# Optimization experiments

Hardware: AMD Instinct MI355X
Metric: run time of the kernel (lower is better)

## Reference

```python
import jax, jax.numpy as jnp
import numpy as np


def setup_inputs() -> dict:
    key = jax.random.key(0)
    k1, k2, k3, k4, k5 = jax.random.split(key, 5)
    B, D, T = 32, 256, 32       # batch, word_feature_dim, seq_len
    Dh, H, Wd = 128, 128, 128   # image_feature_dim, height, width
    word_features = jax.random.normal(k1, (B, D, T), dtype=jnp.float32)
    image_features = jax.random.normal(k2, (B, Dh, H, Wd), dtype=jnp.float32)
    words_mask = jax.random.randint(k3, (B, T), 0, 2, dtype=jnp.int32)
    W = jax.random.normal(k4, (Dh, D), dtype=jnp.float32) * (1.0 / np.sqrt(D))
    b = jax.random.normal(k5, (Dh,), dtype=jnp.float32) * 0.01
    return {"word_features": word_features, "image_features": image_features,
            "words_mask": words_mask, "W": W, "b": b}


def reference(word_features, image_features, words_mask, W, b):
    B, D, T = word_features.shape
    Dh = image_features.shape[1]
    N = image_features.shape[2] * image_features.shape[3]  # H*W
    # values = fc(word_features^T)^T : [B, Dh, T]
    values = jnp.einsum('bdt,kd->bkt', word_features, W) + b[None, :, None]
    # queries: [B, N, Dh] (flatten spatial)
    queries = image_features.reshape(B, Dh, N)
    # scores S: [B, N, T]
    S = jnp.einsum('bkn,bkt->bnt', queries, values)
    mask = (words_mask != 0)[:, None, :]  # [B,1,T], True => masked
    S = jnp.where(mask, -jnp.inf, S)
    # softmax over seq dim (original: exp / sum(exp)); stable form is same math
    attn_coefficients = jax.nn.softmax(S, axis=2)  # [B, N, T]
    # context vectors: [B, Dh, N]
    attn = jnp.einsum('bkt,bnt->bkn', values, attn_coefficients)
    return attn, attn_coefficients
```

## Files before the change

### kernel.cpp

```cpp
#include <hip/hip_runtime.h>
#include <math.h>

constexpr int Bc  = 32;
constexpr int Dc  = 256;
constexpr int Tc  = 32;
constexpr int DHc = 128;
constexpr int Nc  = 16384;

__global__ __launch_bounds__(256) void values_kernel(
    const float* __restrict__ wf, const float* __restrict__ Wm,
    const float* __restrict__ bias, float* __restrict__ values)
{
    int id = blockIdx.x * 256 + threadIdx.x;
    int t = id & (Tc - 1);
    int k = (id >> 5) & (DHc - 1);
    int b = id >> 12;
    const float* wrow = Wm + (size_t)k * Dc;
    const float* wfp  = wf + (size_t)b * Dc * Tc + t;
    float acc = bias[k];
    #pragma unroll 8
    for (int d = 0; d < Dc; ++d)
        acc = fmaf(wrow[d], wfp[(size_t)d * Tc], acc);
    values[id] = acc;
}

__global__ __launch_bounds__(256) void attn_kernel(
    const float* __restrict__ img, const float* __restrict__ values,
    const int* __restrict__ mask, float* __restrict__ attn,
    float* __restrict__ coeff)
{
    __shared__ float Vs[DHc * Tc];
    __shared__ float mneg[Tc];

    const int tid  = threadIdx.x;
    const int b    = blockIdx.x >> 5;
    const int tile = blockIdx.x & 31;

    {
        const float4* vg = (const float4*)(values + (size_t)b * DHc * Tc);
        float4* vs = (float4*)Vs;
        #pragma unroll
        for (int i = 0; i < 4; ++i) vs[i * 256 + tid] = vg[i * 256 + tid];
    }
    if (tid < Tc) mneg[tid] = mask[b * Tc + tid] ? -INFINITY : 0.0f;
    __syncthreads();

    const int n = tile * 512 + tid * 2;
    const float* qp = img + (size_t)b * DHc * Nc + n;

    float s0[Tc], s1[Tc];
    #pragma unroll
    for (int t = 0; t < Tc; ++t) { s0[t] = 0.0f; s1[t] = 0.0f; }

    #pragma unroll 2
    for (int k = 0; k < DHc; ++k) {
        const float2 q = *(const float2*)(qp + (size_t)k * Nc);
        const float4* vrow = (const float4*)(Vs + k * Tc);
        #pragma unroll
        for (int tt = 0; tt < 8; ++tt) {
            const float4 v = vrow[tt];
            s0[4*tt+0] = fmaf(q.x, v.x, s0[4*tt+0]);
            s0[4*tt+1] = fmaf(q.x, v.y, s0[4*tt+1]);
            s0[4*tt+2] = fmaf(q.x, v.z, s0[4*tt+2]);
            s0[4*tt+3] = fmaf(q.x, v.w, s0[4*tt+3]);
            s1[4*tt+0] = fmaf(q.y, v.x, s1[4*tt+0]);
            s1[4*tt+1] = fmaf(q.y, v.y, s1[4*tt+1]);
            s1[4*tt+2] = fmaf(q.y, v.z, s1[4*tt+2]);
            s1[4*tt+3] = fmaf(q.y, v.w, s1[4*tt+3]);
        }
    }

    float m0 = -INFINITY, m1 = -INFINITY;
    #pragma unroll
    for (int t = 0; t < Tc; ++t) {
        s0[t] += mneg[t]; s1[t] += mneg[t];
        m0 = fmaxf(m0, s0[t]); m1 = fmaxf(m1, s1[t]);
    }
    float sum0 = 0.0f, sum1 = 0.0f;
    #pragma unroll
    for (int t = 0; t < Tc; ++t) {
        s0[t] = __expf(s0[t] - m0); sum0 += s0[t];
        s1[t] = __expf(s1[t] - m1); sum1 += s1[t];
    }
    const float inv0 = 1.0f / sum0, inv1 = 1.0f / sum1;
    #pragma unroll
    for (int t = 0; t < Tc; ++t) { s0[t] *= inv0; s1[t] *= inv1; }

    {
        float4* cp = (float4*)(coeff + ((size_t)b * Nc + n) * Tc);
        #pragma unroll
        for (int tt = 0; tt < 8; ++tt)
            cp[tt] = make_float4(s0[4*tt+0], s0[4*tt+1], s0[4*tt+2], s0[4*tt+3]);
        #pragma unroll
        for (int tt = 0; tt < 8; ++tt)
            cp[8+tt] = make_float4(s1[4*tt+0], s1[4*tt+1], s1[4*tt+2], s1[4*tt+3]);
    }

    float* ap = attn + (size_t)b * DHc * Nc + n;
    #pragma unroll 2
    for (int k = 0; k < DHc; ++k) {
        const float4* vrow = (const float4*)(Vs + k * Tc);
        float a0 = 0.f, b0 = 0.f, c0 = 0.f, d0 = 0.f;
        float a1 = 0.f, b1 = 0.f, c1 = 0.f, d1 = 0.f;
        #pragma unroll
        for (int tt = 0; tt < 8; ++tt) {
            const float4 v = vrow[tt];
            a0 = fmaf(v.x, s0[4*tt+0], a0);
            b0 = fmaf(v.y, s0[4*tt+1], b0);
            c0 = fmaf(v.z, s0[4*tt+2], c0);
            d0 = fmaf(v.w, s0[4*tt+3], d0);
            a1 = fmaf(v.x, s1[4*tt+0], a1);
            b1 = fmaf(v.y, s1[4*tt+1], b1);
            c1 = fmaf(v.z, s1[4*tt+2], c1);
            d1 = fmaf(v.w, s1[4*tt+3], d1);
        }
        *(float2*)(ap + (size_t)k * Nc) =
            make_float2((a0 + b0) + (c0 + d0), (a1 + b1) + (c1 + d1));
    }
}

extern "C" void kernel_launch(void* const* d_in, const int* in_sizes, int n_in,
                              void* d_out, int out_size, void* d_ws, size_t ws_size,
                              hipStream_t stream)
{
    const float* wf   = (const float*)d_in[0];
    const float* img  = (const float*)d_in[1];
    const int*   msk  = (const int*)d_in[2];
    const float* Wm   = (const float*)d_in[3];
    const float* bias = (const float*)d_in[4];

    float* attn  = (float*)d_out;
    float* coeff = attn + (size_t)Bc * DHc * Nc;
    float* vals  = (float*)d_ws;

    values_kernel<<<(Bc * DHc * Tc) / 256, 256, 0, stream>>>(wf, Wm, bias, vals);
    attn_kernel<<<(Bc * Nc) / 512, 256, 0, stream>>>(img, vals, msk, attn, coeff);
}
```

Baseline: 611.6 us.

## Read values via uniform scalar loads instead of LDS and prefetch query rows

```diff
diff --git a/kernel.cpp b/kernel.cpp
--- a/kernel.cpp
+++ b/kernel.cpp
@@ -24,58 +24,74 @@
     values[id] = acc;
 }
 
-__global__ __launch_bounds__(256) void attn_kernel(
+__global__ __launch_bounds__(256, 4) void attn_kernel(
     const float* __restrict__ img, const float* __restrict__ values,
     const int* __restrict__ mask, float* __restrict__ attn,
     float* __restrict__ coeff)
 {
-    __shared__ float Vs[DHc * Tc];
-    __shared__ float mneg[Tc];
-
     const int tid  = threadIdx.x;
     const int b    = blockIdx.x >> 5;
     const int tile = blockIdx.x & 31;
+    const int n    = tile * 512 + tid * 2;
 
-    {
-        const float4* vg = (const float4*)(values + (size_t)b * DHc * Tc);
-        float4* vs = (float4*)Vs;
-        #pragma unroll
-        for (int i = 0; i < 4; ++i) vs[i * 256 + tid] = vg[i * 256 + tid];
-    }
-    if (tid < Tc) mneg[tid] = mask[b * Tc + tid] ? -INFINITY : 0.0f;
-    __syncthreads();
+    const float* __restrict__ vb = values + (size_t)b * DHc * Tc;
+    const float* __restrict__ qp = img + (size_t)b * DHc * Nc + n;
 
-    const int n = tile * 512 + tid * 2;
-    const float* qp = img + (size_t)b * DHc * Nc + n;
+    unsigned mbits = 0u;
+    #pragma unroll
+    for (int t = 0; t < Tc; ++t)
+        mbits |= mask[b * Tc + t] ? (1u << t) : 0u;
 
     float s0[Tc], s1[Tc];
     #pragma unroll
     for (int t = 0; t < Tc; ++t) { s0[t] = 0.0f; s1[t] = 0.0f; }
 
-    #pragma unroll 2
-    for (int k = 0; k < DHc; ++k) {
-        const float2 q = *(const float2*)(qp + (size_t)k * Nc);
-        const float4* vrow = (const float4*)(Vs + k * Tc);
+    float2 qA[4], qB[4];
+    #pragma unroll
+    for (int j = 0; j < 4; ++j) qA[j] = *(const float2*)(qp + (size_t)j * Nc);
+
+    for (int c = 0; c < 32; c += 2) {
         #pragma unroll
-        for (int tt = 0; tt < 8; ++tt) {
-            const float4 v = vrow[tt];
-            s0[4*tt+0] = fmaf(q.x, v.x, s0[4*tt+0]);
-            s0[4*tt+1] = fmaf(q.x, v.y, s0[4*tt+1]);
-            s0[4*tt+2] = fmaf(q.x, v.z, s0[4*tt+2]);
-            s0[4*tt+3] = fmaf(q.x, v.w, s0[4*tt+3]);
-            s1[4*tt+0] = fmaf(q.y, v.x, s1[4*tt+0]);
-            s1[4*tt+1] = fmaf(q.y, v.y, s1[4*tt+1]);
-            s1[4*tt+2] = fmaf(q.y, v.z, s1[4*tt+2]);
-            s1[4*tt+3] = fmaf(q.y, v.w, s1[4*tt+3]);
+        for (int j = 0; j < 4; ++j)
+            qB[j] = *(const float2*)(qp + (size_t)((c + 1) * 4 + j) * Nc);
+        #pragma unroll
+        for (int j = 0; j < 4; ++j) {
+            const int k = c * 4 + j;
+            const float2 q = qA[j];
+            const float* vr = vb + k * Tc;
+            #pragma unroll
+            for (int t = 0; t < Tc; ++t) {
+                const float v = vr[t];
+                s0[t] = fmaf(q.x, v, s0[t]);
+                s1[t] = fmaf(q.y, v, s1[t]);
+            }
+        }
+        if (c + 2 < 32) {
+            #pragma unroll
+            for (int j = 0; j < 4; ++j)
+                qA[j] = *(const float2*)(qp + (size_t)((c + 2) * 4 + j) * Nc);
+        }
+        #pragma unroll
+        for (int j = 0; j < 4; ++j) {
+            const int k = (c + 1) * 4 + j;
+            const float2 q = qB[j];
+            const float* vr = vb + k * Tc;
+            #pragma unroll
+            for (int t = 0; t < Tc; ++t) {
+                const float v = vr[t];
+                s0[t] = fmaf(q.x, v, s0[t]);
+                s1[t] = fmaf(q.y, v, s1[t]);
+            }
         }
     }
 
+    #pragma unroll
+    for (int t = 0; t < Tc; ++t)
+        if (mbits & (1u << t)) { s0[t] = -INFINITY; s1[t] = -INFINITY; }
+
     float m0 = -INFINITY, m1 = -INFINITY;
     #pragma unroll
-    for (int t = 0; t < Tc; ++t) {
-        s0[t] += mneg[t]; s1[t] += mneg[t];
-        m0 = fmaxf(m0, s0[t]); m1 = fmaxf(m1, s1[t]);
-    }
+    for (int t = 0; t < Tc; ++t) { m0 = fmaxf(m0, s0[t]); m1 = fmaxf(m1, s1[t]); }
     float sum0 = 0.0f, sum1 = 0.0f;
     #pragma unroll
     for (int t = 0; t < Tc; ++t) {
@@ -99,20 +115,21 @@
     float* ap = attn + (size_t)b * DHc * Nc + n;
     #pragma unroll 2
     for (int k = 0; k < DHc; ++k) {
-        const float4* vrow = (const float4*)(Vs + k * Tc);
+        const float* vr = vb + k * Tc;
         float a0 = 0.f, b0 = 0.f, c0 = 0.f, d0 = 0.f;
         float a1 = 0.f, b1 = 0.f, c1 = 0.f, d1 = 0.f;
         #pragma unroll
         for (int tt = 0; tt < 8; ++tt) {
-            const float4 v = vrow[tt];
-            a0 = fmaf(v.x, s0[4*tt+0], a0);
-            b0 = fmaf(v.y, s0[4*tt+1], b0);
-            c0 = fmaf(v.z, s0[4*tt+2], c0);
-            d0 = fmaf(v.w, s0[4*tt+3], d0);
-            a1 = fmaf(v.x, s1[4*tt+0], a1);
-            b1 = fmaf(v.y, s1[4*tt+1], b1);
-            c1 = fmaf(v.z, s1[4*tt+2], c1);
-            d1 = fmaf(v.w, s1[4*tt+3], d1);
+            const float vx = vr[4*tt+0], vy = vr[4*tt+1];
+            const float vz = vr[4*tt+2], vw = vr[4*tt+3];
+            a0 = fmaf(vx, s0[4*tt+0], a0);
+            b0 = fmaf(vy, s0[4*tt+1], b0);
+            c0 = fmaf(vz, s0[4*tt+2], c0);
+            d0 = fmaf(vw, s0[4*tt+3], d0);
+            a1 = fmaf(vx, s1[4*tt+0], a1);
+            b1 = fmaf(vy, s1[4*tt+1], b1);
+            c1 = fmaf(vz, s1[4*tt+2], c1);
+            d1 = fmaf(vw, s1[4*tt+3], d1);
         }
         *(float2*)(ap + (size_t)k * Nc) =
             make_float2((a0 + b0) + (c0 + d0), (a1 + b1) + (c1 + d1));
```

Measured after the change: 712.7 us. +16.5%, slower.
